# Kernel optimization log

Measured on AMD Instinct MI355X. Metric: run time of the kernel, lower is better.

The kernel has to match this reference:

```python
import jax, jax.numpy as jnp
import numpy as np
import math

B, T, H, D = 4, 2048, 16, 64
C = H * D            # d_model = 1024
FF = 4096            # mlp_hidden_dim
N_LAYERS = 12
EPS = 1e-5


def setup_inputs() -> dict:
    key = jax.random.key(0)
    ks = jax.random.split(key, 8)
    res_scale = 1.0 / math.sqrt(2 * N_LAYERS)
    std_c = math.sqrt(2.0 / C)
    std_ff = math.sqrt(2.0 / FF)
    return {
        "x": jax.random.normal(ks[0], (B, T, C), jnp.float32),
        "ln1_w": jnp.ones((C,), jnp.float32),
        "ln1_b": jnp.zeros((C,), jnp.float32),
        # weights stored [in, out] (transposed vs torch nn.Linear.weight)
        "w_qkv": jax.random.normal(ks[1], (C, 3 * C), jnp.float32) * std_c,
        "b_qkv": jnp.zeros((3 * C,), jnp.float32),
        "w_o": jax.random.normal(ks[2], (C, C), jnp.float32) * std_c * res_scale,
        "b_o": jnp.zeros((C,), jnp.float32),
        "ln2_w": jnp.ones((C,), jnp.float32),
        "ln2_b": jnp.zeros((C,), jnp.float32),
        "w_fc": jax.random.normal(ks[3], (C, FF), jnp.float32) * std_c,
        "b_fc": jnp.zeros((FF,), jnp.float32),
        "w_out": jax.random.normal(ks[4], (FF, C), jnp.float32) * std_ff * res_scale,
        "b_out": jnp.zeros((C,), jnp.float32),
    }


def _layer_norm(x, w, b):
    m = jnp.mean(x, axis=-1, keepdims=True)
    v = jnp.mean(jnp.square(x - m), axis=-1, keepdims=True)
    return (x - m) * jax.lax.rsqrt(v + EPS) * w + b


def reference(x, ln1_w, ln1_b, w_qkv, b_qkv, w_o, b_o, ln2_w, ln2_b, w_fc, b_fc, w_out, b_out):
    Bx, Tx, Cx = x.shape
    # attention
    qkv = _layer_norm(x, ln1_w, ln1_b) @ w_qkv + b_qkv          # [B,T,3C]
    q, k, v = jnp.split(qkv, 3, axis=-1)
    q = q.reshape(Bx, Tx, H, D)
    k = k.reshape(Bx, Tx, H, D)
    v = v.reshape(Bx, Tx, H, D)
    att = jnp.einsum("bqhd,bkhd->bhqk", q, k) / math.sqrt(D)    # [B,H,T,T]
    mask = jnp.tril(jnp.ones((Tx, Tx), dtype=bool))
    att = jnp.where(mask, att, -jnp.inf)
    att = jax.nn.softmax(att, axis=-1)
    y = jnp.einsum("bhqk,bkhd->bqhd", att, v).reshape(Bx, Tx, Cx)
    x = x + y @ w_o + b_o
    # mlp (torch F.gelu default = exact erf gelu)
    h = jax.nn.gelu(_layer_norm(x, ln2_w, ln2_b) @ w_fc + b_fc, approximate=False)
    x = x + h @ w_out + b_out
    return x
```

## Files before the change

### kernel.cpp

```cpp
#include <hip/hip_runtime.h>
#include <hip/hip_bf16.h>
#include <cstdint>


#define B_ 4
#define T_ 2048
#define H_ 16
#define D_ 64
#define C_ 1024
#define FF_ 4096
#define M_ (B_ * T_)
#define QKV_N (3 * C_)

typedef __bf16 bf16x8 __attribute__((ext_vector_type(8)));
typedef __bf16 bf16x4 __attribute__((ext_vector_type(4)));
typedef float floatx4 __attribute__((ext_vector_type(4)));

#define MFMA16(a, b, c) __builtin_amdgcn_mfma_f32_16x16x32_bf16(a, b, c, 0, 0, 0)

__device__ __forceinline__ void gload16(const void* g, void* l) {
  __builtin_amdgcn_global_load_lds(
      (const __attribute__((address_space(1))) void*)g,
      (__attribute__((address_space(3))) void*)l, 16, 0, 0);
}

__device__ __forceinline__ void lds_fence() {
  asm volatile("s_waitcnt lgkmcnt(0)" ::: "memory");
}

__device__ __forceinline__ float gelu_f(float v) {
  return 0.5f * v * (1.0f + erff(v * 0.70710678118654752f));
}

__global__ __launch_bounds__(256) void convert_transpose(
    const float* __restrict__ w, __bf16* __restrict__ wt, int K, int N) {
  __shared__ float tile[32][33];
  const int n0 = blockIdx.x * 32, k0 = blockIdx.y * 32;
  const int tx = threadIdx.x & 31, ty = threadIdx.x >> 5;
#pragma unroll
  for (int i = 0; i < 4; ++i)
    tile[ty + i * 8][tx] = w[(size_t)(k0 + ty + i * 8) * N + n0 + tx];
  __syncthreads();
#pragma unroll
  for (int i = 0; i < 4; ++i)
    wt[(size_t)(n0 + ty + i * 8) * K + k0 + tx] = (__bf16)tile[tx][ty + i * 8];
}

__global__ __launch_bounds__(256) void ln_kernel(
    const float* __restrict__ x, const float* __restrict__ w,
    const float* __restrict__ b, __bf16* __restrict__ out) {
  __shared__ float red[4];
  const int row = blockIdx.x, tid = threadIdx.x;
  const float4 v = ((const float4*)(x + (size_t)row * C_))[tid];
  float s = v.x + v.y + v.z + v.w;
#pragma unroll
  for (int off = 1; off < 64; off <<= 1) s += __shfl_xor(s, off, 64);
  if ((tid & 63) == 0) red[tid >> 6] = s;
  __syncthreads();
  const float mean = (red[0] + red[1] + red[2] + red[3]) * (1.0f / C_);
  __syncthreads();
  const float dx = v.x - mean, dy = v.y - mean, dz = v.z - mean, dw = v.w - mean;
  float s2 = dx * dx + dy * dy + dz * dz + dw * dw;
#pragma unroll
  for (int off = 1; off < 64; off <<= 1) s2 += __shfl_xor(s2, off, 64);
  if ((tid & 63) == 0) red[tid >> 6] = s2;
  __syncthreads();
  const float var = (red[0] + red[1] + red[2] + red[3]) * (1.0f / C_);
  const float rstd = rsqrtf(var + 1e-5f);
  const float4 wv = ((const float4*)w)[tid];
  const float4 bv = ((const float4*)b)[tid];
  bf16x4 o;
  o[0] = (__bf16)(dx * rstd * wv.x + bv.x);
  o[1] = (__bf16)(dy * rstd * wv.y + bv.y);
  o[2] = (__bf16)(dz * rstd * wv.z + bv.z);
  o[3] = (__bf16)(dw * rstd * wv.w + bv.w);
  *(bf16x4*)(out + (size_t)row * C_ + tid * 4) = o;
}


template <bool GELU, bool RESID, bool OUTBF16>
__global__ __launch_bounds__(256, 2) void gemm_kernel(
    const __bf16* __restrict__ A, const __bf16* __restrict__ BT,
    const float* __restrict__ bias, const float* __restrict__ resid,
    float* __restrict__ outF, __bf16* __restrict__ outB, int M, int N, int K) {
  __shared__ __bf16 As[128 * 64];
  __shared__ __bf16 Bs[128 * 64];
  const int tid = threadIdx.x;
  const int wave = tid >> 6, lane = tid & 63;
  const int lane15 = lane & 15, quad = lane >> 4;
  const int r7 = lane15 & 7;

  const int gx = gridDim.x, gy = gridDim.y;
  const int linear = blockIdx.y * gx + blockIdx.x;
  const int xcd = linear & 7, idx = linear >> 3;
  const int bn = idx % gx;
  const int bm = xcd * (gy >> 3) + idx / gx;

  const int m0 = bm * 128, n0 = bn * 128;
  const int wm = (wave >> 1) * 64, wn = (wave & 1) * 64;

  const int srow = lane >> 3;
  const int gc8 = (lane & 7) ^ srow;

  floatx4 acc[4][4] = {};

  for (int k0 = 0; k0 < K; k0 += 64) {
#pragma unroll
    for (int t = 0; t < 4; ++t) {
      const int row = wave * 32 + t * 8;
      gload16(A + (size_t)(m0 + row + srow) * K + k0 + gc8 * 8, &As[row * 64]);
      gload16(BT + (size_t)(n0 + row + srow) * K + k0 + gc8 * 8, &Bs[row * 64]);
    }
    __syncthreads();
#pragma unroll
    for (int kk8 = 0; kk8 < 8; kk8 += 4) {
      bf16x8 af[4], bfr[4];
#pragma unroll
      for (int i = 0; i < 4; ++i) {
        af[i] = *(const bf16x8*)
            &As[(wm + i * 16 + lane15) * 64 + (((kk8 + quad) ^ r7) << 3)];
        bfr[i] = *(const bf16x8*)
            &Bs[(wn + i * 16 + lane15) * 64 + (((kk8 + quad) ^ r7) << 3)];
      }
#pragma unroll
      for (int i = 0; i < 4; ++i)
#pragma unroll
        for (int j = 0; j < 4; ++j) acc[i][j] = MFMA16(af[i], bfr[j], acc[i][j]);
    }
    __syncthreads();
  }

#pragma unroll
  for (int mi = 0; mi < 4; ++mi) {
    const int row = m0 + wm + mi * 16 + quad * 4;
#pragma unroll
    for (int ni = 0; ni < 4; ++ni) {
      const int col = n0 + wn + ni * 16 + lane15;
      const float bsum = bias[col];
#pragma unroll
      for (int r = 0; r < 4; ++r) {
        const size_t idx2 = (size_t)(row + r) * N + col;
        float v = acc[mi][ni][r] + bsum;
        if (GELU) v = gelu_f(v);
        if (RESID) v += resid[idx2];
        if (OUTBF16) outB[idx2] = (__bf16)v;
        else outF[idx2] = v;
      }
    }
  }
}

template <bool GELU, bool RESID, bool OUTBF16>
__global__ __launch_bounds__(256, 4) void gemm_n64_kernel(
    const __bf16* __restrict__ A, const __bf16* __restrict__ BT,
    const float* __restrict__ bias, const float* __restrict__ resid,
    float* __restrict__ outF, __bf16* __restrict__ outB, int M, int N, int K) {
  __shared__ __bf16 As[128 * 64];
  __shared__ __bf16 Bs[64 * 64];
  const int tid = threadIdx.x;
  const int wave = tid >> 6, lane = tid & 63;
  const int lane15 = lane & 15, quad = lane >> 4;
  const int r7 = lane15 & 7;

  const int gx = gridDim.x, gy = gridDim.y;
  const int linear = blockIdx.y * gx + blockIdx.x;
  const int xcd = linear & 7, idx = linear >> 3;
  const int bn = idx % gx;
  const int bm = xcd * (gy >> 3) + idx / gx;

  const int m0 = bm * 128, n0 = bn * 64;
  const int wm = (wave >> 1) * 64, wn = (wave & 1) * 32;

  const int srow = lane >> 3;
  const int gc8 = (lane & 7) ^ srow;

  floatx4 acc[4][2] = {};

  for (int k0 = 0; k0 < K; k0 += 64) {
#pragma unroll
    for (int t = 0; t < 4; ++t) {
      const int row = wave * 32 + t * 8;
      gload16(A + (size_t)(m0 + row + srow) * K + k0 + gc8 * 8, &As[row * 64]);
    }
    {
      const int row = wave * 16 + (lane >> 3 & 8) + ((lane >> 3) & 7);
    }
#pragma unroll
    for (int t = 0; t < 2; ++t) {
      const int row = wave * 16 + t * 8;
      gload16(BT + (size_t)(n0 + row + srow) * K + k0 + gc8 * 8, &Bs[row * 64]);
    }
    __syncthreads();
#pragma unroll
    for (int kk8 = 0; kk8 < 8; kk8 += 4) {
      bf16x8 af[4], bfr[2];
#pragma unroll
      for (int i = 0; i < 4; ++i)
        af[i] = *(const bf16x8*)
            &As[(wm + i * 16 + lane15) * 64 + (((kk8 + quad) ^ r7) << 3)];
#pragma unroll
      for (int j = 0; j < 2; ++j)
        bfr[j] = *(const bf16x8*)
            &Bs[(wn + j * 16 + lane15) * 64 + (((kk8 + quad) ^ r7) << 3)];
#pragma unroll
      for (int i = 0; i < 4; ++i)
#pragma unroll
        for (int j = 0; j < 2; ++j) acc[i][j] = MFMA16(af[i], bfr[j], acc[i][j]);
    }
    __syncthreads();
  }

#pragma unroll
  for (int mi = 0; mi < 4; ++mi) {
    const int row = m0 + wm + mi * 16 + quad * 4;
#pragma unroll
    for (int ni = 0; ni < 2; ++ni) {
      const int col = n0 + wn + ni * 16 + lane15;
      const float bsum = bias[col];
#pragma unroll
      for (int r = 0; r < 4; ++r) {
        const size_t idx2 = (size_t)(row + r) * N + col;
        float v = acc[mi][ni][r] + bsum;
        if (GELU) v = gelu_f(v);
        if (RESID) v += resid[idx2];
        if (OUTBF16) outB[idx2] = (__bf16)v;
        else outF[idx2] = v;
      }
    }
  }
}

#define PT_S 72
#define VT_S 72
__global__ __launch_bounds__(256, 4) void attn_kernel(
    const __bf16* __restrict__ qkv, __bf16* __restrict__ y) {
  const int linear = blockIdx.x;
  const int xcd = linear & 7, idx = linear >> 3;
  const int pair = idx & 15;
  const int bh = xcd * 8 + (idx >> 4);
  const int b = bh >> 4, h = bh & 15;

  const int tid = threadIdx.x, wave = tid >> 6, lane = tid & 63;
  const int lane15 = lane & 15, quad = lane >> 4;
  __shared__ __bf16 K0[2][64 * 32];
  __shared__ __bf16 K1[2][64 * 32];
  __shared__ __bf16 Vt[64 * VT_S];
  __shared__ __bf16 Pt[4][16 * PT_S];

  const int krow_loc = lane >> 2;
  const int kdc = (lane & 3) * 8;
  const int v_kv = tid & 63;
  const int v_d0 = (tid >> 6) * 16;
  const float QSCALE = 0.125f * 1.44269504088896f;

  const int qt_of[2] = {pair, 31 - pair};

  bf16x8 onesf;
#pragma unroll
  for (int j = 0; j < 8; ++j) onesf[j] = (__bf16)1.0f;

  bf16x8 vr0, vr1;
  int g = 0;

  {
    const size_t gk =
        (size_t)(b * T_ + wave * 16 + krow_loc) * QKV_N + C_ + h * 64 + kdc;
    gload16(qkv + gk, &K0[0][wave * 16 * 32]);
    gload16(qkv + gk + 32, &K1[0][wave * 16 * 32]);
    const __bf16* vsrc =
        qkv + (size_t)(b * T_ + v_kv) * QKV_N + 2 * C_ + h * 64 + v_d0;
    vr0 = *(const bf16x8*)vsrc;
    vr1 = *(const bf16x8*)(vsrc + 8);
  }

#pragma unroll
  for (int seg = 0; seg < 2; ++seg) {
    const int qt = qt_of[seg];
    const int qrow0 = qt * 64 + wave * 16;

    bf16x8 qf0, qf1;
    {
      const size_t base =
          (size_t)(b * T_ + qrow0 + lane15) * QKV_N + h * 64 + quad * 8;
      const bf16x8 r0 = *(const bf16x8*)(qkv + base);
      const bf16x8 r1 = *(const bf16x8*)(qkv + base + 32);
#pragma unroll
      for (int j = 0; j < 8; ++j) {
        qf0[j] = (__bf16)((float)r0[j] * QSCALE);
        qf1[j] = (__bf16)((float)r1[j] * QSCALE);
      }
    }

    floatx4 o[4] = {};
    floatx4 o4 = {0.f, 0.f, 0.f, 0.f};

    const int ntiles = qt + 1;
    for (int kvt = 0; kvt < ntiles; ++kvt) {
      const int buf = g & 1;
      const int c0 = kvt * 64;
      __syncthreads();
#pragma unroll
      for (int j = 0; j < 8; ++j) {
        Vt[(v_d0 + j) * VT_S + v_kv] = vr0[j];
        Vt[(v_d0 + 8 + j) * VT_S + v_kv] = vr1[j];
      }
      __syncthreads();

      if (!(seg == 1 && kvt + 1 >= ntiles)) {
        const int nkvt = (kvt + 1 >= ntiles) ? 0 : kvt + 1;
        const int nc0 = nkvt * 64;
        const int nbuf = (g + 1) & 1;
        const size_t gk = (size_t)(b * T_ + nc0 + wave * 16 + krow_loc) * QKV_N +
                          C_ + h * 64 + kdc;
        gload16(qkv + gk, &K0[nbuf][wave * 16 * 32]);
        gload16(qkv + gk + 32, &K1[nbuf][wave * 16 * 32]);
        const __bf16* vsrc = qkv + (size_t)(b * T_ + nc0 + v_kv) * QKV_N +
                             2 * C_ + h * 64 + v_d0;
        vr0 = *(const bf16x8*)vsrc;
        vr1 = *(const bf16x8*)(vsrc + 8);
      }

      float p[4][4];
#pragma unroll
      for (int nt = 0; nt < 4; ++nt) {
        const bf16x8 kf0 =
            *(const bf16x8*)&K0[buf][(nt * 16 + lane15) * 32 + quad * 8];
        const bf16x8 kf1 =
            *(const bf16x8*)&K1[buf][(nt * 16 + lane15) * 32 + quad * 8];
        floatx4 s = {0.f, 0.f, 0.f, 0.f};
        s = MFMA16(qf0, kf0, s);
        s = MFMA16(qf1, kf1, s);
#pragma unroll
        for (int r = 0; r < 4; ++r) p[nt][r] = s[r];
      }
      if (kvt == qt) {
#pragma unroll
        for (int nt = 0; nt < 4; ++nt) {
          const int tk = c0 + nt * 16 + lane15;
#pragma unroll
          for (int r = 0; r < 4; ++r) {
            const int tq = qrow0 + quad * 4 + r;
            p[nt][r] = (tk <= tq) ? p[nt][r] : -1e30f;
          }
        }
      }

#pragma unroll
      for (int nt = 0; nt < 4; ++nt)
#pragma unroll
        for (int r = 0; r < 4; ++r)
          Pt[wave][(quad * 4 + r) * PT_S + nt * 16 + lane15] =
              (__bf16)__builtin_amdgcn_exp2f(p[nt][r]);
      lds_fence();

#pragma unroll
      for (int half = 0; half < 2; ++half) {
        const bf16x8 pf =
            *(const bf16x8*)&Pt[wave][lane15 * PT_S + half * 32 + quad * 8];
#pragma unroll
        for (int dt = 0; dt < 4; ++dt) {
          const bf16x8 vf =
              *(const bf16x8*)&Vt[(dt * 16 + lane15) * VT_S + half * 32 + quad * 8];
          o[dt] = MFMA16(pf, vf, o[dt]);
        }
        o4 = MFMA16(pf, onesf, o4);
      }
      ++g;
    }

#pragma unroll
    for (int r = 0; r < 4; ++r) {
      const int tq = qrow0 + quad * 4 + r;
      const float inv = 1.0f / o4[r];
#pragma unroll
      for (int dt = 0; dt < 4; ++dt)
        y[(size_t)(b * T_ + tq) * C_ + h * 64 + dt * 16 + lane15] =
            (__bf16)(o[dt][r] * inv);
    }
  }
}

extern "C" void kernel_launch(void* const* d_in, const int* in_sizes, int n_in,
                              void* d_out, int out_size, void* d_ws,
                              size_t ws_size, hipStream_t stream) {
  const float* x     = (const float*)d_in[0];
  const float* ln1_w = (const float*)d_in[1];
  const float* ln1_b = (const float*)d_in[2];
  const float* w_qkv = (const float*)d_in[3];
  const float* b_qkv = (const float*)d_in[4];
  const float* w_o   = (const float*)d_in[5];
  const float* b_o   = (const float*)d_in[6];
  const float* ln2_w = (const float*)d_in[7];
  const float* ln2_b = (const float*)d_in[8];
  const float* w_fc  = (const float*)d_in[9];
  const float* b_fc  = (const float*)d_in[10];
  const float* w_out = (const float*)d_in[11];
  const float* b_out = (const float*)d_in[12];

  char* ws = (char*)d_ws;
  __bf16* wqkvT = (__bf16*)(ws + 0);
  __bf16* woT   = (__bf16*)(ws + 6291456);
  __bf16* wfcT  = (__bf16*)(ws + 8388608);
  __bf16* woutT = (__bf16*)(ws + 16777216);
  __bf16* xn    = (__bf16*)(ws + 25165824);
  __bf16* qkv   = (__bf16*)(ws + 41943040);
  __bf16* yb    = (__bf16*)(ws + 92274688);
  float*  x1    = (float*)(ws + 109051904);
  __bf16* hb    = (__bf16*)(ws + 142606336);

  convert_transpose<<<dim3(QKV_N / 32, C_ / 32), 256, 0, stream>>>(w_qkv, wqkvT, C_, QKV_N);
  convert_transpose<<<dim3(C_ / 32, C_ / 32), 256, 0, stream>>>(w_o, woT, C_, C_);
  convert_transpose<<<dim3(FF_ / 32, C_ / 32), 256, 0, stream>>>(w_fc, wfcT, C_, FF_);
  convert_transpose<<<dim3(C_ / 32, FF_ / 32), 256, 0, stream>>>(w_out, woutT, FF_, C_);

  ln_kernel<<<M_, 256, 0, stream>>>(x, ln1_w, ln1_b, xn);
  gemm_kernel<false, false, true><<<dim3(QKV_N / 128, M_ / 128), 256, 0, stream>>>(
      xn, wqkvT, b_qkv, nullptr, nullptr, qkv, M_, QKV_N, C_);
  attn_kernel<<<1024, 256, 0, stream>>>(qkv, yb);
  gemm_n64_kernel<false, true, false><<<dim3(C_ / 64, M_ / 128), 256, 0, stream>>>(
      yb, woT, b_o, x, x1, nullptr, M_, C_, C_);
  ln_kernel<<<M_, 256, 0, stream>>>(x1, ln2_w, ln2_b, xn);
  gemm_kernel<true, false, true><<<dim3(FF_ / 128, M_ / 128), 256, 0, stream>>>(
      xn, wfcT, b_fc, nullptr, nullptr, hb, M_, FF_, C_);
  gemm_n64_kernel<false, true, false><<<dim3(C_ / 64, M_ / 128), 256, 0, stream>>>(
      hb, woutT, b_out, x1, (float*)d_out, nullptr, M_, C_, FF_);
}
```

Before: 521.5 us.

## Use tanh-style GELU approximation, grouped GEMM tile swizzle, and vectorized attention LDS writes

Replaces the exact erf GELU with a sigmoid/exp2-based tanh approximation to cut transcendental cost in the FC epilogue. Changes the GEMM block-to-tile mapping to a grouped swizzle so concurrently running blocks share B tiles for better L2 reuse. In attention, swaps the MFMA operand order so each lane holds four consecutive keys, which lets P be written to LDS as packed bf16x4. V is transposed with paired 32-bit LDS stores instead of scalar bf16 stores. The GELU approximation departs from the exact erf form the reference uses and may add error.

```diff
diff --git a/kernel.cpp b/kernel.cpp
--- a/kernel.cpp
+++ b/kernel.cpp
@@ -28,8 +28,12 @@
   asm volatile("s_waitcnt lgkmcnt(0)" ::: "memory");
 }
 
-__device__ __forceinline__ float gelu_f(float v) {
-  return 0.5f * v * (1.0f + erff(v * 0.70710678118654752f));
+__device__ __forceinline__ float gelu_f(float x) {
+  const float k1 = 2.3021178518f;
+  const float ck = 0.1029410426f;
+  const float y = x * __builtin_fmaf(x * x, ck, k1);
+  const float t = __builtin_amdgcn_exp2f(y);
+  return x - x * __builtin_amdgcn_rcpf(t + 1.0f);
 }
 
 __global__ __launch_bounds__(256) void convert_transpose(
@@ -77,6 +81,15 @@
   *(bf16x4*)(out + (size_t)row * C_ + tid * 4) = o;
 }
 
+__device__ __forceinline__ void swizzle_mn(int gx, int gy, int* bm, int* bn) {
+  const int linear = blockIdx.y * gx + blockIdx.x;
+  const int xcd = linear & 7, idx = linear >> 3;
+  const int band = gy >> 3;
+  const int per_grp = band * 8;
+  const int g = idx / per_grp, rem = idx % per_grp;
+  *bm = xcd * band + rem % band;
+  *bn = g * 8 + rem / band;
+}
 
 template <bool GELU, bool RESID, bool OUTBF16>
 __global__ __launch_bounds__(256, 2) void gemm_kernel(
@@ -90,12 +103,8 @@
   const int lane15 = lane & 15, quad = lane >> 4;
   const int r7 = lane15 & 7;
 
-  const int gx = gridDim.x, gy = gridDim.y;
-  const int linear = blockIdx.y * gx + blockIdx.x;
-  const int xcd = linear & 7, idx = linear >> 3;
-  const int bn = idx % gx;
-  const int bm = xcd * (gy >> 3) + idx / gx;
-
+  int bm, bn;
+  swizzle_mn(gridDim.x, gridDim.y, &bm, &bn);
   const int m0 = bm * 128, n0 = bn * 128;
   const int wm = (wave >> 1) * 64, wn = (wave & 1) * 64;
 
@@ -162,12 +171,8 @@
   const int lane15 = lane & 15, quad = lane >> 4;
   const int r7 = lane15 & 7;
 
-  const int gx = gridDim.x, gy = gridDim.y;
-  const int linear = blockIdx.y * gx + blockIdx.x;
-  const int xcd = linear & 7, idx = linear >> 3;
-  const int bn = idx % gx;
-  const int bm = xcd * (gy >> 3) + idx / gx;
-
+  int bm, bn;
+  swizzle_mn(gridDim.x, gridDim.y, &bm, &bn);
   const int m0 = bm * 128, n0 = bn * 64;
   const int wm = (wave >> 1) * 64, wn = (wave & 1) * 32;
 
@@ -181,9 +186,6 @@
     for (int t = 0; t < 4; ++t) {
       const int row = wave * 32 + t * 8;
       gload16(A + (size_t)(m0 + row + srow) * K + k0 + gc8 * 8, &As[row * 64]);
-    }
-    {
-      const int row = wave * 16 + (lane >> 3 & 8) + ((lane >> 3) & 7);
     }
 #pragma unroll
     for (int t = 0; t < 2; ++t) {
@@ -249,8 +251,8 @@
 
   const int krow_loc = lane >> 2;
   const int kdc = (lane & 3) * 8;
-  const int v_kv = tid & 63;
-  const int v_d0 = (tid >> 6) * 16;
+  const int v_kvp = tid & 31;
+  const int v_dgrp = tid >> 5;
   const float QSCALE = 0.125f * 1.44269504088896f;
 
   const int qt_of[2] = {pair, 31 - pair};
@@ -267,16 +269,17 @@
         (size_t)(b * T_ + wave * 16 + krow_loc) * QKV_N + C_ + h * 64 + kdc;
     gload16(qkv + gk, &K0[0][wave * 16 * 32]);
     gload16(qkv + gk + 32, &K1[0][wave * 16 * 32]);
-    const __bf16* vsrc =
-        qkv + (size_t)(b * T_ + v_kv) * QKV_N + 2 * C_ + h * 64 + v_d0;
+    const __bf16* vsrc = qkv + (size_t)(b * T_ + 2 * v_kvp) * QKV_N +
+                         2 * C_ + h * 64 + v_dgrp * 8;
     vr0 = *(const bf16x8*)vsrc;
-    vr1 = *(const bf16x8*)(vsrc + 8);
+    vr1 = *(const bf16x8*)(vsrc + QKV_N);
   }
 
 #pragma unroll
   for (int seg = 0; seg < 2; ++seg) {
     const int qt = qt_of[seg];
     const int qrow0 = qt * 64 + wave * 16;
+    const int tq = qrow0 + lane15;
 
     bf16x8 qf0, qf1;
     {
@@ -301,8 +304,10 @@
       __syncthreads();
 #pragma unroll
       for (int j = 0; j < 8; ++j) {
-        Vt[(v_d0 + j) * VT_S + v_kv] = vr0[j];
-        Vt[(v_d0 + 8 + j) * VT_S + v_kv] = vr1[j];
+        union { __bf16 hh[2]; uint32_t u; } pk;
+        pk.hh[0] = vr0[j];
+        pk.hh[1] = vr1[j];
+        *(uint32_t*)&Vt[(v_dgrp * 8 + j) * VT_S + 2 * v_kvp] = pk.u;
       }
       __syncthreads();
 
@@ -314,13 +319,12 @@
                           C_ + h * 64 + kdc;
         gload16(qkv + gk, &K0[nbuf][wave * 16 * 32]);
         gload16(qkv + gk + 32, &K1[nbuf][wave * 16 * 32]);
-        const __bf16* vsrc = qkv + (size_t)(b * T_ + nc0 + v_kv) * QKV_N +
-                             2 * C_ + h * 64 + v_d0;
+        const __bf16* vsrc = qkv + (size_t)(b * T_ + nc0 + 2 * v_kvp) * QKV_N +
+                             2 * C_ + h * 64 + v_dgrp * 8;
         vr0 = *(const bf16x8*)vsrc;
-        vr1 = *(const bf16x8*)(vsrc + 8);
-      }
-
-      float p[4][4];
+        vr1 = *(const bf16x8*)(vsrc + QKV_N);
+      }
+
 #pragma unroll
       for (int nt = 0; nt < 4; ++nt) {
         const bf16x8 kf0 =
@@ -328,29 +332,23 @@
         const bf16x8 kf1 =
             *(const bf16x8*)&K1[buf][(nt * 16 + lane15) * 32 + quad * 8];
         floatx4 s = {0.f, 0.f, 0.f, 0.f};
-        s = MFMA16(qf0, kf0, s);
-        s = MFMA16(qf1, kf1, s);
-#pragma unroll
-        for (int r = 0; r < 4; ++r) p[nt][r] = s[r];
-      }
-      if (kvt == qt) {
-#pragma unroll
-        for (int nt = 0; nt < 4; ++nt) {
-          const int tk = c0 + nt * 16 + lane15;
+        s = MFMA16(kf0, qf0, s);
+        s = MFMA16(kf1, qf1, s);
+        const int tk0 = c0 + nt * 16 + quad * 4;
+        bf16x4 pk4;
+        if (kvt == qt) {
 #pragma unroll
           for (int r = 0; r < 4; ++r) {
-            const int tq = qrow0 + quad * 4 + r;
-            p[nt][r] = (tk <= tq) ? p[nt][r] : -1e30f;
+            const float sv = (tk0 + r <= tq) ? s[r] : -1e30f;
+            pk4[r] = (__bf16)__builtin_amdgcn_exp2f(sv);
           }
+        } else {
+#pragma unroll
+          for (int r = 0; r < 4; ++r)
+            pk4[r] = (__bf16)__builtin_amdgcn_exp2f(s[r]);
         }
-      }
-
-#pragma unroll
-      for (int nt = 0; nt < 4; ++nt)
-#pragma unroll
-        for (int r = 0; r < 4; ++r)
-          Pt[wave][(quad * 4 + r) * PT_S + nt * 16 + lane15] =
-              (__bf16)__builtin_amdgcn_exp2f(p[nt][r]);
+        *(bf16x4*)&Pt[wave][lane15 * PT_S + nt * 16 + quad * 4] = pk4;
+      }
       lds_fence();
 
 #pragma unroll
@@ -370,11 +368,11 @@
 
 #pragma unroll
     for (int r = 0; r < 4; ++r) {
-      const int tq = qrow0 + quad * 4 + r;
+      const int tqo = qrow0 + quad * 4 + r;
       const float inv = 1.0f / o4[r];
 #pragma unroll
       for (int dt = 0; dt < 4; ++dt)
-        y[(size_t)(b * T_ + tq) * C_ + h * 64 + dt * 16 + lane15] =
+        y[(size_t)(b * T_ + tqo) * C_ + h * 64 + dt * 16 + lane15] =
             (__bf16)(o[dt][r] * inv);
     }
   }
```

Result: faster. 476.3 us (-8.7%).
